# Optimization experiments

Hardware: AMD Instinct MI355X
Metric: run time of the kernel (lower is better)

## Reference

```python
import jax, jax.numpy as jnp
import numpy as np

D_MODEL = 1024
DIM = 128

def setup_inputs() -> dict:
    key = jax.random.key(0)
    k1, k2, k3 = jax.random.split(key, 3)
    x = jax.random.normal(k1, (4, 4096, D_MODEL), dtype=jnp.float32)
    # nn.Linear(d_model, 3*dim): weight [3*dim, d_model] in torch; store as [d_model, 3*dim]
    W_qkv = jax.random.normal(k2, (D_MODEL, 3 * DIM), dtype=jnp.float32) * (D_MODEL ** -0.5)
    b_qkv = jax.random.normal(k3, (3 * DIM,), dtype=jnp.float32) * 0.01
    return {"x": x, "W_qkv": W_qkv, "b_qkv": b_qkv}

def reference(x, W_qkv, b_qkv):
    # qkv projection: [b, t, 3*dim]
    qkv = jnp.einsum('btd,de->bte', x, W_qkv) + b_qkv
    # split 'b t (d n)' with n=3 -> q, k, v each [b, t, dim]
    b, t, _ = qkv.shape
    qkv = qkv.reshape(b, t, DIM, 3)
    q, k, v = qkv[..., 0], qkv[..., 1], qkv[..., 2]
    scale = DIM ** -0.5
    scores = jnp.einsum('btd,bsd->bts', q, k) * scale  # [b, t, t]
    attn = jax.nn.softmax(scores, axis=-1)
    return jnp.einsum('bts,bsd->btd', attn, v)
```

## Files before the change

kernel.cpp:

```cpp
#include <hip/hip_runtime.h>
#include <hip/hip_bf16.h>

using short8 = __attribute__((ext_vector_type(8))) short;
using f32x4  = __attribute__((ext_vector_type(4))) float;

#define MFMA16(a,b,c) __builtin_amdgcn_mfma_f32_16x16x32_bf16(a,b,c,0,0,0)

__device__ __forceinline__ unsigned short bf16r(float f) {
  unsigned u = __builtin_bit_cast(unsigned, f);
  return (unsigned short)((u + 0x7fffu + ((u >> 16) & 1u)) >> 16);
}

__device__ __forceinline__ short8 cvt8(f32x4 lo, f32x4 hi) {
  union { short8 s; unsigned u[4]; } v;
  asm("v_cvt_pk_bf16_f32 %0, %1, %2" : "=v"(v.u[0]) : "v"(lo[0]), "v"(lo[1]));
  asm("v_cvt_pk_bf16_f32 %0, %1, %2" : "=v"(v.u[1]) : "v"(lo[2]), "v"(lo[3]));
  asm("v_cvt_pk_bf16_f32 %0, %1, %2" : "=v"(v.u[2]) : "v"(hi[0]), "v"(hi[1]));
  asm("v_cvt_pk_bf16_f32 %0, %1, %2" : "=v"(v.u[3]) : "v"(hi[2]), "v"(hi[3]));
  return v.s;
}

template <typename T>
__device__ __forceinline__ void load_lds16(const T* g, T* l) {
  __builtin_amdgcn_global_load_lds((const __attribute__((address_space(1))) unsigned*)g,
                                   (__attribute__((address_space(3))) unsigned*)l, 16, 0, 0);
}

constexpr int TB = 4;
constexpr int TT = 4096;
constexpr int DM = 1024;
constexpr int DD = 128;
constexpr int NE = 384;
constexpr int NSPLIT = 4;
constexpr int CHUNK = TT / NSPLIT;
constexpr float QSCALE = 0.12751744f;

__global__ void wtrans_kernel(const float* __restrict__ W, unsigned short* __restrict__ Wt) {
  int i = blockIdx.x * 256 + threadIdx.x;
  int k = i / NE, n = i - k * NE;
  Wt[n * DM + k] = bf16r(W[i]);
}

__global__ __launch_bounds__(256, 4)
void qkv_kernel(const float* __restrict__ x, const unsigned short* __restrict__ Wt,
                const float* __restrict__ bq,
                unsigned short* __restrict__ Qb, unsigned short* __restrict__ Kb,
                unsigned short* __restrict__ Vt) {
  const int tid = threadIdx.x;
  const int wid = tid >> 6, lane = tid & 63;
  const int g = lane >> 4, c = lane & 15;
  const int wr = wid >> 1, wc = wid & 1;
  const int m0 = blockIdx.x * 64;
  const int n0 = blockIdx.y * 128;

  __shared__ float          As[2][2048];
  __shared__ unsigned short Bs[2][4096];

  f32x4 acc[2][4];
  #pragma unroll
  for (int m = 0; m < 2; ++m)
    #pragma unroll
    for (int n = 0; n < 4; ++n) acc[m][n] = f32x4{0.f, 0.f, 0.f, 0.f};

#define QKV_STAGE(buf, kb) do {                                                  \
    _Pragma("unroll")                                                            \
    for (int i_ = 0; i_ < 2; ++i_) {                                             \
      int L = i_ * 256 + tid, ar = L >> 3, au = (L & 7) ^ (ar & 7);              \
      load_lds16(x + (size_t)(m0 + ar) * DM + (kb) * 32 + au * 4,                \
                 &As[buf][L * 4]);                                               \
    }                                                                            \
    _Pragma("unroll")                                                            \
    for (int i_ = 0; i_ < 2; ++i_) {                                             \
      int L = i_ * 256 + tid, br = L >> 2, bu = (L & 3) ^ (br & 3);              \
      load_lds16(Wt + (size_t)(n0 + br) * DM + (kb) * 32 + bu * 8,               \
                 &Bs[buf][L * 8]);                                               \
    }                                                                            \
  } while (0)

  QKV_STAGE(0, 0);
  __syncthreads();

  const int cx7 = (c & 7) << 4, cx3 = (c & 3) << 4;
  for (int kb = 0; kb < DM / 32; ++kb) {
    const int cur = kb & 1;
    if (kb + 1 < DM / 32) QKV_STAGE(cur ^ 1, kb + 1);

    short8 a[2], b[4];
    #pragma unroll
    for (int m = 0; m < 2; ++m) {
      int row = wr * 32 + m * 16 + c;
      f32x4 lo = *(const f32x4*)((const char*)&As[cur][0] + row * 128 + ((g * 32)      ^ cx7));
      f32x4 hi = *(const f32x4*)((const char*)&As[cur][0] + row * 128 + ((g * 32 + 16) ^ cx7));
      a[m] = cvt8(lo, hi);
    }
    #pragma unroll
    for (int n = 0; n < 4; ++n) {
      int row = wc * 64 + n * 16 + c;
      b[n] = *(const short8*)((const char*)&Bs[cur][0] + row * 64 + ((g * 16) ^ cx3));
    }

    __builtin_amdgcn_s_setprio(1);
    #pragma unroll
    for (int m = 0; m < 2; ++m)
      #pragma unroll
      for (int n = 0; n < 4; ++n)
        acc[m][n] = MFMA16(a[m], b[n], acc[m][n]);
    __builtin_amdgcn_s_setprio(0);

    __syncthreads();
  }

  #pragma unroll
  for (int n = 0; n < 4; ++n) {
    int e = n0 + wc * 64 + n * 16 + c;
    float bias = bq[e];
    int n3 = e % 3, d = e / 3;
    #pragma unroll
    for (int m = 0; m < 2; ++m) {
      #pragma unroll
      for (int r = 0; r < 4; ++r) {
        int row = m0 + wr * 32 + m * 16 + g * 4 + r;
        float val = acc[m][n][r] + bias;
        int bb = row >> 12, tr = row & (TT - 1);
        if (n3 == 0)      Qb[row * DD + d] = bf16r(val * QSCALE);
        else if (n3 == 1) Kb[row * DD + d] = bf16r(val);
        else              Vt[(bb * DD + d) * TT + tr] = bf16r(val);
      }
    }
  }
#undef QKV_STAGE
}

constexpr int KVB = 64;
__global__ __launch_bounds__(256, 2)
void attn_kernel(const unsigned short* __restrict__ Qb, const unsigned short* __restrict__ Kb,
                 const unsigned short* __restrict__ Vt,
                 float* __restrict__ Opart, float* __restrict__ Mpart, float* __restrict__ Lpart) {
  const int tid = threadIdx.x;
  const int wid = tid >> 6, lane = tid & 63;
  const int g = lane >> 4, c = lane & 15;
  const int b = blockIdx.y;
  const int z = blockIdx.z;
  const int qw = blockIdx.x * 128 + wid * 32;
  const int s_base = z * CHUNK;

  __shared__ __align__(16) unsigned char KtS[KVB * 256];
  __shared__ __align__(16) unsigned char VtS[128 * 128];
  __shared__ __align__(16) unsigned char PlS[4][32 * 128];

  const int cx = (c & 7) << 4;

  short8 qf[2][4];
  #pragma unroll
  for (int grp = 0; grp < 2; ++grp) {
    const unsigned short* qrow = Qb + (size_t)(b * TT + qw + grp * 16 + c) * DD + g * 8;
    #pragma unroll
    for (int kk = 0; kk < 4; ++kk) qf[grp][kk] = *(const short8*)(qrow + kk * 32);
  }

  short8 onesb;
  #pragma unroll
  for (int j = 0; j < 8; ++j) onesb[j] = (short)0x3F80;

  float mr[2][4];
  f32x4 lacc[2];
  f32x4 oacc[2][8];
  #pragma unroll
  for (int grp = 0; grp < 2; ++grp) {
    #pragma unroll
    for (int r = 0; r < 4; ++r) mr[grp][r] = -1e30f;
    lacc[grp] = f32x4{0.f, 0.f, 0.f, 0.f};
    #pragma unroll
    for (int n = 0; n < 8; ++n) oacc[grp][n] = f32x4{0.f, 0.f, 0.f, 0.f};
  }

  short8 kreg[4], vreg[4];
  const int krow_ = tid >> 4;
  const int kgcol = (tid & 15) * 8;
  const int kwb   = ((tid & 15) * 16) ^ ((krow_ & 7) << 4);
  const int vrow_ = tid >> 3;
  const int vgcol = (tid & 7) * 8;
  const int vwb   = ((tid & 7) * 16) ^ ((vrow_ & 7) << 4);

  const unsigned short* Kbase = Kb + (size_t)(b * TT) * DD;
  const unsigned short* Vbase = Vt + (size_t)(b * DD) * TT;

  #pragma unroll
  for (int p = 0; p < 4; ++p) {
    kreg[p] = *(const short8*)(Kbase + (size_t)(s_base + p * 16 + krow_) * DD + kgcol);
    vreg[p] = *(const short8*)(Vbase + (size_t)(p * 32 + vrow_) * TT + s_base + vgcol);
  }
  #pragma unroll
  for (int p = 0; p < 4; ++p) {
    *(short8*)(KtS + (p * 16 + krow_) * 256 + kwb) = kreg[p];
    *(short8*)(VtS + (p * 32 + vrow_) * 128 + vwb) = vreg[p];
  }
  __syncthreads();

  const int NT = CHUNK / KVB;
  for (int it = 0; it < NT; ++it) {
    if (it + 1 < NT) {
      int s0 = s_base + (it + 1) * KVB;
      #pragma unroll
      for (int p = 0; p < 4; ++p) {
        kreg[p] = *(const short8*)(Kbase + (size_t)(s0 + p * 16 + krow_) * DD + kgcol);
        vreg[p] = *(const short8*)(Vbase + (size_t)(p * 32 + vrow_) * TT + s0 + vgcol);
      }
    }

    f32x4 sacc[2][4];
    #pragma unroll
    for (int grp = 0; grp < 2; ++grp)
      #pragma unroll
      for (int t = 0; t < 4; ++t) sacc[grp][t] = f32x4{0.f, 0.f, 0.f, 0.f};
    __builtin_amdgcn_s_setprio(1);
    #pragma unroll
    for (int kk = 0; kk < 4; ++kk) {
      #pragma unroll
      for (int t = 0; t < 4; ++t) {
        short8 kf = *(const short8*)(KtS + (t * 16 + c) * 256 + ((kk * 64 + g * 16) ^ cx));
        sacc[0][t] = MFMA16(qf[0][kk], kf, sacc[0][t]);
        sacc[1][t] = MFMA16(qf[1][kk], kf, sacc[1][t]);
      }
    }
    __builtin_amdgcn_s_setprio(0);

    #pragma unroll
    for (int grp = 0; grp < 2; ++grp) {
      float pe[4][4];
      #pragma unroll
      for (int r = 0; r < 4; ++r) {
        float mx = fmaxf(fmaxf(sacc[grp][0][r], sacc[grp][1][r]),
                         fmaxf(sacc[grp][2][r], sacc[grp][3][r]));
        mx = fmaxf(mx, __shfl_xor(mx, 1));
        mx = fmaxf(mx, __shfl_xor(mx, 2));
        mx = fmaxf(mx, __shfl_xor(mx, 4));
        mx = fmaxf(mx, __shfl_xor(mx, 8));
        float mnew = fmaxf(mr[grp][r], mx);
        float alpha = exp2f(mr[grp][r] - mnew);
        mr[grp][r] = mnew;
        #pragma unroll
        for (int t = 0; t < 4; ++t) pe[t][r] = exp2f(sacc[grp][t][r] - mnew);
        lacc[grp][r] *= alpha;
        #pragma unroll
        for (int n = 0; n < 8; ++n) oacc[grp][n][r] *= alpha;
      }
      #pragma unroll
      for (int t = 0; t < 4; ++t)
        #pragma unroll
        for (int r = 0; r < 4; ++r) {
          int prow = grp * 16 + g * 4 + r;
          *(unsigned short*)(PlS[wid] + prow * 128 + ((t * 32 + c * 2) ^ (((g * 4 + r) & 7) << 4)))
              = bf16r(pe[t][r]);
        }
    }

    __builtin_amdgcn_s_setprio(1);
    #pragma unroll
    for (int ks = 0; ks < 2; ++ks) {
      short8 pf0 = *(const short8*)(PlS[wid] + (c) * 128      + ((ks * 64 + g * 16) ^ cx));
      short8 pf1 = *(const short8*)(PlS[wid] + (16 + c) * 128 + ((ks * 64 + g * 16) ^ cx));
      lacc[0] = MFMA16(pf0, onesb, lacc[0]);
      lacc[1] = MFMA16(pf1, onesb, lacc[1]);
      #pragma unroll
      for (int n = 0; n < 8; ++n) {
        short8 vf = *(const short8*)(VtS + (n * 16 + c) * 128 + ((ks * 64 + g * 16) ^ cx));
        oacc[0][n] = MFMA16(pf0, vf, oacc[0][n]);
        oacc[1][n] = MFMA16(pf1, vf, oacc[1][n]);
      }
    }
    __builtin_amdgcn_s_setprio(0);

    __syncthreads();
    if (it + 1 < NT) {
      #pragma unroll
      for (int p = 0; p < 4; ++p) {
        *(short8*)(KtS + (p * 16 + krow_) * 256 + kwb) = kreg[p];
        *(short8*)(VtS + (p * 32 + vrow_) * 128 + vwb) = vreg[p];
      }
    }
    __syncthreads();
  }

  const size_t pbase = (size_t)(z * TB + b) * TT;
  #pragma unroll
  for (int grp = 0; grp < 2; ++grp) {
    #pragma unroll
    for (int n = 0; n < 8; ++n)
      #pragma unroll
      for (int r = 0; r < 4; ++r) {
        int row = qw + grp * 16 + g * 4 + r;
        Opart[(pbase + row) * DD + n * 16 + c] = oacc[grp][n][r];
      }
    if (c == 0) {
      #pragma unroll
      for (int r = 0; r < 4; ++r) {
        int row = qw + grp * 16 + g * 4 + r;
        Mpart[pbase + row] = mr[grp][r];
        Lpart[pbase + row] = lacc[grp][r];
      }
    }
  }
}

__global__ void merge_kernel(const float* __restrict__ Opart, const float* __restrict__ Mpart,
                             const float* __restrict__ Lpart, float* __restrict__ out) {
  int i = blockIdx.x * 256 + threadIdx.x;
  int grow = i >> 5, d4 = (i & 31) << 2;
  float m[NSPLIT];
  float ms = -1e30f;
  #pragma unroll
  for (int s = 0; s < NSPLIT; ++s) { m[s] = Mpart[s * (TB * TT) + grow]; ms = fmaxf(ms, m[s]); }
  float w[NSPLIT];
  float denom = 0.f;
  #pragma unroll
  for (int s = 0; s < NSPLIT; ++s) {
    w[s] = exp2f(m[s] - ms);
    denom += w[s] * Lpart[s * (TB * TT) + grow];
  }
  float rd = 1.0f / denom;
  f32x4 o = {0.f, 0.f, 0.f, 0.f};
  #pragma unroll
  for (int s = 0; s < NSPLIT; ++s) {
    f32x4 v = *(const f32x4*)(Opart + (size_t)(s * (TB * TT) + grow) * DD + d4);
    o += v * w[s];
  }
  *(f32x4*)(out + (size_t)grow * DD + d4) = o * rd;
}

extern "C" void kernel_launch(void* const* d_in, const int* in_sizes, int n_in,
                              void* d_out, int out_size, void* d_ws, size_t ws_size,
                              hipStream_t stream) {
  const float* x  = (const float*)d_in[0];
  const float* W  = (const float*)d_in[1];
  const float* bq = (const float*)d_in[2];
  float* out = (float*)d_out;

  unsigned char* ws = (unsigned char*)d_ws;
  unsigned short* Qb = (unsigned short*)(ws);
  unsigned short* Kb = (unsigned short*)(ws + (4u  << 20));
  unsigned short* Vt = (unsigned short*)(ws + (8u  << 20));
  unsigned short* Wt = (unsigned short*)(ws + (12u << 20));
  float* Mpart = (float*)(ws + (13u << 20));
  float* Lpart = (float*)(ws + (14u << 20));
  float* Opart = (float*)(ws + (16u << 20));

  wtrans_kernel<<<(DM * NE) / 256, 256, 0, stream>>>(W, Wt);
  qkv_kernel<<<dim3(TB * TT / 64, NE / 128), 256, 0, stream>>>(x, Wt, bq, Qb, Kb, Vt);
  attn_kernel<<<dim3(TT / 128, TB, NSPLIT), 256, 0, stream>>>(Qb, Kb, Vt, Opart, Mpart, Lpart);
  merge_kernel<<<(TB * TT * 32) / 256, 256, 0, stream>>>(Opart, Mpart, Lpart, out);
}
```

Baseline: 212.0 us.

## Pre-cast x to bf16, deepen QKV K-tile, add lazy softmax rescale

Adds a separate kernel that converts x to bf16 once, so the QKV GEMM loads bf16 tiles with a 64-wide K step and drops the in-loop float-to-bf16 conversion. The attention kernel now skips rescaling the output accumulators when no row max grows by more than 8 (log2 units) across the wavefront. Launch bounds change for both kernels. In exchange there is an extra full pass over x through global memory, xb reuses the Opart workspace region (safe only because qkv finishes before attn writes Opart), and skipping the rescale lets exp values reach up to 2^8, which bf16 P values must tolerate.

```diff
diff --git a/kernel.cpp b/kernel.cpp
--- a/kernel.cpp
+++ b/kernel.cpp
@@ -35,14 +35,21 @@
 constexpr int CHUNK = TT / NSPLIT;
 constexpr float QSCALE = 0.12751744f;
 
+__global__ void xcast_kernel(const float* __restrict__ x, unsigned short* __restrict__ xb) {
+  int i = blockIdx.x * 256 + threadIdx.x;
+  f32x4 lo = *(const f32x4*)(x + (size_t)i * 8);
+  f32x4 hi = *(const f32x4*)(x + (size_t)i * 8 + 4);
+  *(short8*)(xb + (size_t)i * 8) = cvt8(lo, hi);
+}
+
 __global__ void wtrans_kernel(const float* __restrict__ W, unsigned short* __restrict__ Wt) {
   int i = blockIdx.x * 256 + threadIdx.x;
   int k = i / NE, n = i - k * NE;
   Wt[n * DM + k] = bf16r(W[i]);
 }
 
-__global__ __launch_bounds__(256, 4)
-void qkv_kernel(const float* __restrict__ x, const unsigned short* __restrict__ Wt,
+__global__ __launch_bounds__(256, 3)
+void qkv_kernel(const unsigned short* __restrict__ xb, const unsigned short* __restrict__ Wt,
                 const float* __restrict__ bq,
                 unsigned short* __restrict__ Qb, unsigned short* __restrict__ Kb,
                 unsigned short* __restrict__ Vt) {
@@ -53,8 +60,8 @@
   const int m0 = blockIdx.x * 64;
   const int n0 = blockIdx.y * 128;
 
-  __shared__ float          As[2][2048];
-  __shared__ unsigned short Bs[2][4096];
+  __shared__ unsigned short As[2][64 * 64];
+  __shared__ unsigned short Bs[2][128 * 64];
 
   f32x4 acc[2][4];
   #pragma unroll
@@ -65,14 +72,14 @@
 #define QKV_STAGE(buf, kb) do {                                                  \
     _Pragma("unroll")                                                            \
     for (int i_ = 0; i_ < 2; ++i_) {                                             \
-      int L = i_ * 256 + tid, ar = L >> 3, au = (L & 7) ^ (ar & 7);              \
-      load_lds16(x + (size_t)(m0 + ar) * DM + (kb) * 32 + au * 4,                \
-                 &As[buf][L * 4]);                                               \
+      int L = i_ * 256 + tid, r_ = L >> 3, u_ = (L & 7) ^ (r_ & 7);              \
+      load_lds16(xb + (size_t)(m0 + r_) * DM + (kb) * 64 + u_ * 8,               \
+                 &As[buf][L * 8]);                                               \
     }                                                                            \
     _Pragma("unroll")                                                            \
-    for (int i_ = 0; i_ < 2; ++i_) {                                             \
-      int L = i_ * 256 + tid, br = L >> 2, bu = (L & 3) ^ (br & 3);              \
-      load_lds16(Wt + (size_t)(n0 + br) * DM + (kb) * 32 + bu * 8,               \
+    for (int i_ = 0; i_ < 4; ++i_) {                                             \
+      int L = i_ * 256 + tid, r_ = L >> 3, u_ = (L & 7) ^ (r_ & 7);              \
+      load_lds16(Wt + (size_t)(n0 + r_) * DM + (kb) * 64 + u_ * 8,               \
                  &Bs[buf][L * 8]);                                               \
     }                                                                            \
   } while (0)
@@ -80,31 +87,35 @@
   QKV_STAGE(0, 0);
   __syncthreads();
 
-  const int cx7 = (c & 7) << 4, cx3 = (c & 3) << 4;
-  for (int kb = 0; kb < DM / 32; ++kb) {
+  const int cx = (c & 7) << 4;
+  for (int kb = 0; kb < DM / 64; ++kb) {
     const int cur = kb & 1;
-    if (kb + 1 < DM / 32) QKV_STAGE(cur ^ 1, kb + 1);
-
-    short8 a[2], b[4];
+    if (kb + 1 < DM / 64) QKV_STAGE(cur ^ 1, kb + 1);
+
+    short8 a[2][2], b[4][2];
     #pragma unroll
     for (int m = 0; m < 2; ++m) {
       int row = wr * 32 + m * 16 + c;
-      f32x4 lo = *(const f32x4*)((const char*)&As[cur][0] + row * 128 + ((g * 32)      ^ cx7));
-      f32x4 hi = *(const f32x4*)((const char*)&As[cur][0] + row * 128 + ((g * 32 + 16) ^ cx7));
-      a[m] = cvt8(lo, hi);
+      #pragma unroll
+      for (int kk = 0; kk < 2; ++kk)
+        a[m][kk] = *(const short8*)((const char*)&As[cur][0] + row * 128 + ((kk * 64 + g * 16) ^ cx));
     }
     #pragma unroll
     for (int n = 0; n < 4; ++n) {
       int row = wc * 64 + n * 16 + c;
-      b[n] = *(const short8*)((const char*)&Bs[cur][0] + row * 64 + ((g * 16) ^ cx3));
+      #pragma unroll
+      for (int kk = 0; kk < 2; ++kk)
+        b[n][kk] = *(const short8*)((const char*)&Bs[cur][0] + row * 128 + ((kk * 64 + g * 16) ^ cx));
     }
 
     __builtin_amdgcn_s_setprio(1);
     #pragma unroll
-    for (int m = 0; m < 2; ++m)
-      #pragma unroll
-      for (int n = 0; n < 4; ++n)
-        acc[m][n] = MFMA16(a[m], b[n], acc[m][n]);
+    for (int kk = 0; kk < 2; ++kk)
+      #pragma unroll
+      for (int m = 0; m < 2; ++m)
+        #pragma unroll
+        for (int n = 0; n < 4; ++n)
+          acc[m][n] = MFMA16(a[m][kk], b[n][kk], acc[m][n]);
     __builtin_amdgcn_s_setprio(0);
 
     __syncthreads();
@@ -132,7 +143,7 @@
 }
 
 constexpr int KVB = 64;
-__global__ __launch_bounds__(256, 2)
+__global__ __launch_bounds__(256, 3)
 void attn_kernel(const unsigned short* __restrict__ Qb, const unsigned short* __restrict__ Kb,
                  const unsigned short* __restrict__ Vt,
                  float* __restrict__ Opart, float* __restrict__ Mpart, float* __restrict__ Lpart) {
@@ -225,9 +236,9 @@
     }
     __builtin_amdgcn_s_setprio(0);
 
-    #pragma unroll
-    for (int grp = 0; grp < 2; ++grp) {
-      float pe[4][4];
+    float mxv[2][4];
+    #pragma unroll
+    for (int grp = 0; grp < 2; ++grp)
       #pragma unroll
       for (int r = 0; r < 4; ++r) {
         float mx = fmaxf(fmaxf(sacc[grp][0][r], sacc[grp][1][r]),
@@ -236,14 +247,34 @@
         mx = fmaxf(mx, __shfl_xor(mx, 2));
         mx = fmaxf(mx, __shfl_xor(mx, 4));
         mx = fmaxf(mx, __shfl_xor(mx, 8));
-        float mnew = fmaxf(mr[grp][r], mx);
-        float alpha = exp2f(mr[grp][r] - mnew);
-        mr[grp][r] = mnew;
+        mxv[grp][r] = mx;
+      }
+    float need = -1e30f;
+    #pragma unroll
+    for (int grp = 0; grp < 2; ++grp)
+      #pragma unroll
+      for (int r = 0; r < 4; ++r) need = fmaxf(need, mxv[grp][r] - mr[grp][r]);
+    const bool skip = __all(need <= 8.0f);
+
+    #pragma unroll
+    for (int grp = 0; grp < 2; ++grp) {
+      float pe[4][4];
+      #pragma unroll
+      for (int r = 0; r < 4; ++r) {
+        float mref;
+        if (skip) {
+          mref = mr[grp][r];
+        } else {
+          float mnew = fmaxf(mr[grp][r], mxv[grp][r]);
+          float alpha = exp2f(mr[grp][r] - mnew);
+          mr[grp][r] = mnew;
+          lacc[grp][r] *= alpha;
+          #pragma unroll
+          for (int n = 0; n < 8; ++n) oacc[grp][n][r] *= alpha;
+          mref = mnew;
+        }
         #pragma unroll
-        for (int t = 0; t < 4; ++t) pe[t][r] = exp2f(sacc[grp][t][r] - mnew);
-        lacc[grp][r] *= alpha;
-        #pragma unroll
-        for (int n = 0; n < 8; ++n) oacc[grp][n][r] *= alpha;
+        for (int t = 0; t < 4; ++t) pe[t][r] = exp2f(sacc[grp][t][r] - mref);
       }
       #pragma unroll
       for (int t = 0; t < 4; ++t)
@@ -344,9 +375,11 @@
   float* Mpart = (float*)(ws + (13u << 20));
   float* Lpart = (float*)(ws + (14u << 20));
   float* Opart = (float*)(ws + (16u << 20));
-
+  unsigned short* xb = (unsigned short*)(ws + (16u << 20));
+
+  xcast_kernel<<<(TB * TT * DM) / (8 * 256), 256, 0, stream>>>(x, xb);
   wtrans_kernel<<<(DM * NE) / 256, 256, 0, stream>>>(W, Wt);
-  qkv_kernel<<<dim3(TB * TT / 64, NE / 128), 256, 0, stream>>>(x, Wt, bq, Qb, Kb, Vt);
+  qkv_kernel<<<dim3(TB * TT / 64, NE / 128), 256, 0, stream>>>(xb, Wt, bq, Qb, Kb, Vt);
   attn_kernel<<<dim3(TT / 128, TB, NSPLIT), 256, 0, stream>>>(Qb, Kb, Vt, Opart, Mpart, Lpart);
   merge_kernel<<<(TB * TT * 32) / 256, 256, 0, stream>>>(Opart, Mpart, Lpart, out);
 }
```

Result: slower. 297.9 us (+40.5%).
